# Performance work log

Measured on AMD Instinct MI355X. Metric: run time of the kernel, lower is better.

Reference implementation:

```python
import jax, jax.numpy as jnp
import numpy as np

T_MAX = 20
NUM_HEADS = 8
COMPLEXITY_W = 0.3
LN_EPS = 1e-5


def _layernorm(h, g, b):
    mu = jnp.mean(h, axis=-1, keepdims=True)
    var = jnp.var(h, axis=-1, keepdims=True)
    return (h - mu) / jnp.sqrt(var + LN_EPS) * g + b


def _gate_mlp(x, W1, b1, g, be, W2, b2, W3, b3):
    # Linear -> LayerNorm -> ReLU -> (Dropout=id in eval) -> Linear -> ReLU -> Linear -> Sigmoid
    h = jax.nn.relu(_layernorm(x @ W1 + b1, g, be))
    h = jax.nn.relu(h @ W2 + b2)
    return jax.nn.sigmoid(h @ W3 + b3)


def _adaptive_windows(x, p):
    S = x.shape[1]
    gate = _gate_mlp(x, p['gW1'], p['gb1'], p['gg'], p['gbe'], p['gW2'], p['gb2'], p['gW3'], p['gb3'])
    comp = _gate_mlp(x, p['cW1'], p['cb1'], p['cg'], p['cbe'], p['cW2'], p['cb2'], p['cW3'], p['cb3'])
    pos = jnp.linspace(0.8, 1.2, S, dtype=x.dtype).reshape(1, -1, 1)
    score = ((1.0 - COMPLEXITY_W) * gate + COMPLEXITY_W * comp) * pos
    T_i = jnp.clip(jnp.ceil(score[..., 0] * T_MAX), 1, T_MAX).astype(jnp.int32)  # [B,S]
    return T_i


def _spike_sum(x, T_i, alpha, beta):
    # LIF recurrence over T_MAX steps; accumulate masked spikes. x: [B,S,E]
    z = jnp.zeros_like(x)

    def step(carry, t):
        v, i, acc = carry
        active = (t < T_i).astype(x.dtype)[..., None]  # [B,S,1]
        i = alpha * i + x * active
        v = beta * v + i
        s = (v >= 1.0).astype(x.dtype)
        v = v * (1.0 - s)  # v_reset = 0
        return (v, i, acc + s * active), None

    (_, _, acc), _ = jax.lax.scan(step, (z, z, z), jnp.arange(T_MAX))
    return acc


def _forward(x, params):
    B, S, E = x.shape
    H, D = NUM_HEADS, E // NUM_HEADS
    q = x @ params['Wq']
    k = x @ params['Wk']
    v = x @ params['Wv']
    T_i = _adaptive_windows(x, params)
    q_sum = _spike_sum(q, T_i, params['alpha_q'], params['beta_q'])
    k_sum = _spike_sum(k, T_i, params['alpha_k'], params['beta_k'])
    v_mean = _spike_sum(v, T_i, params['alpha_v'], params['beta_v']) / T_MAX
    q_sum = q_sum.reshape(B, S, H, D)
    k_sum = k_sum.reshape(B, S, H, D)
    v_mean = v_mean.reshape(B, S, H, D)
    scale = D ** -0.5
    scores = jnp.einsum('bihd,bjhd->bhij', q_sum, k_sum) * scale
    w = jax.nn.softmax(scores, axis=-1)
    out = jnp.einsum('bhij,bjhd->bihd', w, v_mean).reshape(B, S, E)
    return out @ params['Wo'] + params['bo']


def setup_inputs() -> dict:
    key = jax.random.key(0)
    ks = iter(jax.random.split(key, 32))
    B, S, E = 4, 1024, 512
    f32 = jnp.float32

    def w(shape, scale=0.02):
        return jax.random.normal(next(ks), shape, dtype=f32) * scale

    inp = {
        'x': jax.random.normal(next(ks), (B, S, E), dtype=f32),
        'Wq': w((E, E)), 'Wk': w((E, E)), 'Wv': w((E, E)),
        'Wo': w((E, E)), 'bo': jnp.zeros((E,), f32),
        'gW1': w((E, 128)), 'gb1': jnp.zeros((128,), f32),
        'gg': jnp.ones((128,), f32), 'gbe': jnp.zeros((128,), f32),
        'gW2': w((128, 64)), 'gb2': jnp.zeros((64,), f32),
        'gW3': w((64, 1)), 'gb3': jnp.zeros((1,), f32),
        'cW1': w((E, 64)), 'cb1': jnp.zeros((64,), f32),
        'cg': jnp.ones((64,), f32), 'cbe': jnp.zeros((64,), f32),
        'cW2': w((64, 32)), 'cb2': jnp.zeros((32,), f32),
        'cW3': w((32, 1)), 'cb3': jnp.zeros((1,), f32),
        'alpha_q': jnp.asarray(np.exp(-1 / 5.0), f32), 'beta_q': jnp.asarray(np.exp(-1 / 20.0), f32),
        'alpha_k': jnp.asarray(np.exp(-1 / 5.0), f32), 'beta_k': jnp.asarray(np.exp(-1 / 20.0), f32),
        'alpha_v': jnp.asarray(np.exp(-1 / 5.0), f32), 'beta_v': jnp.asarray(np.exp(-1 / 20.0), f32),
    }
    return inp


def reference(x, Wq, Wk, Wv, Wo, bo,
              gW1, gb1, gg, gbe, gW2, gb2, gW3, gb3,
              cW1, cb1, cg, cbe, cW2, cb2, cW3, cb3,
              alpha_q, beta_q, alpha_k, beta_k, alpha_v, beta_v):
    params = dict(Wq=Wq, Wk=Wk, Wv=Wv, Wo=Wo, bo=bo,
                  gW1=gW1, gb1=gb1, gg=gg, gbe=gbe, gW2=gW2, gb2=gb2, gW3=gW3, gb3=gb3,
                  cW1=cW1, cb1=cb1, cg=cg, cbe=cbe, cW2=cW2, cb2=cb2, cW3=cW3, cb3=cb3,
                  alpha_q=alpha_q, beta_q=beta_q, alpha_k=alpha_k, beta_k=beta_k,
                  alpha_v=alpha_v, beta_v=beta_v)
    return _forward(x, params)
```

## Files before the change

kernel.cpp:

```cpp
#include <hip/hip_runtime.h>
#include <math.h>

#define SEQ   1024
#define EMB   512
#define NROWS 4096
#define LDP   72
#define GROWS 4

typedef __attribute__((ext_vector_type(8))) short short8;
typedef __attribute__((ext_vector_type(4))) float float4v;

__device__ __forceinline__ float bf2f(unsigned short s) {
    union { float f; unsigned u; } x; x.u = ((unsigned)s) << 16; return x.f;
}
__device__ __forceinline__ unsigned short f2bf(float f) {
    union { float f; unsigned u; } x; x.f = f;
    unsigned r = x.u + 0x7fffu + ((x.u >> 16) & 1u);
    return (unsigned short)(r >> 16);
}

__device__ __forceinline__ void gld16(const unsigned short* g, short* l) {
    __builtin_amdgcn_global_load_lds(
        (__attribute__((address_space(1))) void*)(g),
        (__attribute__((address_space(3))) void*)(l), 16, 0, 0);
}

__device__ __forceinline__ void split3(float x, unsigned short& h, unsigned short& m, unsigned short& l) {
    union { float f; unsigned u; } a; a.f = x;
    const unsigned rh = a.u + 0x7fffu + ((a.u >> 16) & 1u);
    h = (unsigned short)(rh >> 16);
    union { float f; unsigned u; } hf; hf.u = rh & 0xffff0000u;
    const float r1 = x - hf.f;
    a.f = r1;
    const unsigned rm = a.u + 0x7fffu + ((a.u >> 16) & 1u);
    m = (unsigned short)(rm >> 16);
    union { float f; unsigned u; } mf; mf.u = rm & 0xffff0000u;
    const float r2 = r1 - mf.f;
    l = f2bf(r2);
}

template<int H1, int H2>
__device__ __forceinline__ double mlp_eval(
    const double xs[GROWS][EMB], double* h1, double* h2, double* red,
    double* mu_s, double* var_s,
    const float* __restrict__ W1, const float* __restrict__ b1,
    const float* __restrict__ gam, const float* __restrict__ bet,
    const float* __restrict__ W2, const float* __restrict__ b2,
    const float* __restrict__ W3, const float* __restrict__ b3,
    int tid, int myrow)
{
    constexpr int S  = 256 / H1;
    constexpr int KS = EMB / S;

    {
        const int col = tid % H1, sk = tid / H1;
        double acc[GROWS] = {0.0, 0.0, 0.0, 0.0};
        const int kbeg = sk * KS;
        #pragma unroll 4
        for (int k = kbeg; k < kbeg + KS; ++k) {
            const double w = (double)W1[k * H1 + col];
            #pragma unroll
            for (int r = 0; r < GROWS; ++r) acc[r] += w * xs[r][k];
        }
        #pragma unroll
        for (int r = 0; r < GROWS; ++r) red[(sk * GROWS + r) * H1 + col] = acc[r];
    }
    __syncthreads();
    for (int idx = tid; idx < GROWS * H1; idx += 256) {
        const int r = idx / H1, cc = idx % H1;
        double s = 0.0;
        #pragma unroll
        for (int t = 0; t < S; ++t) s += red[(t * GROWS + r) * H1 + cc];
        h1[r * H1 + cc] = s + (double)b1[cc];
    }
    __syncthreads();

    {
        const int w = tid >> 6, l = tid & 63;
        double s = 0.0;
        for (int c = l; c < H1; c += 64) s += h1[w * H1 + c];
        #pragma unroll
        for (int off = 32; off >= 1; off >>= 1) s += __shfl_xor(s, off);
        if (l == 0) mu_s[w] = s / (double)H1;
    }
    __syncthreads();
    {
        const int w = tid >> 6, l = tid & 63;
        const double mu = mu_s[w];
        double s = 0.0;
        for (int c = l; c < H1; c += 64) { const double d = h1[w * H1 + c] - mu; s += d * d; }
        #pragma unroll
        for (int off = 32; off >= 1; off >>= 1) s += __shfl_xor(s, off);
        if (l == 0) var_s[w] = s / (double)H1;
    }
    __syncthreads();
    for (int idx = tid; idx < GROWS * H1; idx += 256) {
        const int r = idx / H1, cc = idx % H1;
        double hn = (h1[r * H1 + cc] - mu_s[r]) / sqrt(var_s[r] + 1e-5) * (double)gam[cc] + (double)bet[cc];
        h1[r * H1 + cc] = hn > 0.0 ? hn : 0.0;
    }
    __syncthreads();

    {
        const int col = tid % H2;
        const int r   = tid / H2;
        if (r < GROWS) {
            double acc = (double)b2[col];
            for (int k = 0; k < H1; ++k)
                acc += (double)W2[k * H2 + col] * h1[r * H1 + k];
            h2[r * H2 + col] = acc > 0.0 ? acc : 0.0;
        }
    }
    __syncthreads();

    {
        const int w = tid >> 6, l = tid & 63;
        double s = 0.0;
        for (int c = l; c < H2; c += 64) s += h2[w * H2 + c] * (double)W3[c];
        #pragma unroll
        for (int off = 32; off >= 1; off >>= 1) s += __shfl_xor(s, off);
        if (l == 0) mu_s[w] = s;
    }
    __syncthreads();
    double ret = 0.0;
    if (myrow >= 0) {
        const double z = mu_s[myrow] + (double)b3[0];
        ret = 1.0 / (1.0 + exp(-z));
    }
    return ret;
}

__global__ __launch_bounds__(256) void gates_split_kernel(
    const float* __restrict__ x,
    const float* __restrict__ gW1, const float* __restrict__ gb1,
    const float* __restrict__ gg,  const float* __restrict__ gbe,
    const float* __restrict__ gW2, const float* __restrict__ gb2,
    const float* __restrict__ gW3, const float* __restrict__ gb3,
    const float* __restrict__ cW1, const float* __restrict__ cb1,
    const float* __restrict__ cg,  const float* __restrict__ cbe,
    const float* __restrict__ cW2, const float* __restrict__ cb2,
    const float* __restrict__ cW3, const float* __restrict__ cb3,
    double* __restrict__ scores)
{
    __shared__ double xs[GROWS][EMB];
    __shared__ double h1[GROWS * 128];
    __shared__ double h2[GROWS * 64];
    __shared__ double red[1024];
    __shared__ double mu_s[GROWS], var_s[GROWS];

    const int row0 = blockIdx.x * GROWS;
    const int tid = threadIdx.x;

    for (int idx = tid; idx < GROWS * EMB; idx += 256) {
        const int r = idx >> 9, cc = idx & 511;
        xs[r][cc] = (double)x[(size_t)(row0 + r) * EMB + cc];
    }
    __syncthreads();

    const int myrow = (tid < GROWS) ? tid : -1;
    double v;
    if (blockIdx.y == 0)
        v = mlp_eval<128, 64>(xs, h1, h2, red, mu_s, var_s,
                              gW1, gb1, gg, gbe, gW2, gb2, gW3, gb3, tid, myrow);
    else
        v = mlp_eval<64, 32>(xs, h1, h2, red, mu_s, var_s,
                             cW1, cb1, cg, cbe, cW2, cb2, cW3, cb3, tid, myrow);

    if (myrow >= 0)
        scores[(size_t)blockIdx.y * NROWS + row0 + myrow] = v;
}

__global__ __launch_bounds__(256) void w_limbs_prep(
    const float* __restrict__ Wq, const float* __restrict__ Wk, const float* __restrict__ Wv,
    unsigned short* __restrict__ WL)
{
    const int z = blockIdx.z;
    const float* __restrict__ W = (z == 0) ? Wq : (z == 1) ? Wk : Wv;
    unsigned short* __restrict__ Th = WL + (size_t)z * 3 * EMB * EMB;
    unsigned short* __restrict__ Tm = Th + (size_t)EMB * EMB;
    unsigned short* __restrict__ Tl = Tm + (size_t)EMB * EMB;

    __shared__ __align__(16) float Ws[64][68];
    const int k0 = blockIdx.y * 64, n0 = blockIdx.x * 64;
    const int t = threadIdx.x;
    #pragma unroll
    for (int it = 0; it < 4; ++it) {
        const int idx = it * 256 + t;
        const int r = idx >> 4, c4 = (idx & 15) * 4;
        *(float4*)&Ws[r][c4] = *(const float4*)&W[(size_t)(k0 + r) * EMB + n0 + c4];
    }
    __syncthreads();
    #pragma unroll
    for (int it = 0; it < 2; ++it) {
        const int idx = it * 256 + t;
        const int n = idx >> 3, k8 = (idx & 7) * 8;
        short8 ph, pm, pl;
        #pragma unroll
        for (int j = 0; j < 8; ++j) {
            unsigned short h, m, l;
            split3(Ws[k8 + j][n], h, m, l);
            ph[j] = (short)h; pm[j] = (short)m; pl[j] = (short)l;
        }
        const size_t o = (size_t)(n0 + n) * EMB + k0 + k8;
        *(short8*)&Th[o] = ph;
        *(short8*)&Tm[o] = pm;
        *(short8*)&Tl[o] = pl;
    }
}

__global__ __launch_bounds__(256) void x_limbs_prep(
    const float* __restrict__ x, unsigned short* __restrict__ XL)
{
    unsigned short* __restrict__ Xh = XL;
    unsigned short* __restrict__ Xm = XL + (size_t)NROWS * EMB;
    unsigned short* __restrict__ Xl = Xm + (size_t)NROWS * EMB;
    const size_t i0 = ((size_t)blockIdx.x * 256 + threadIdx.x) * 8;
    const float4 a0 = *(const float4*)&x[i0];
    const float4 a1 = *(const float4*)&x[i0 + 4];
    const float av8[8] = {a0.x, a0.y, a0.z, a0.w, a1.x, a1.y, a1.z, a1.w};
    short8 ph, pm, pl;
    #pragma unroll
    for (int e = 0; e < 8; ++e) {
        unsigned short h, m, l;
        split3(av8[e], h, m, l);
        ph[e] = (short)h; pm[e] = (short)m; pl[e] = (short)l;
    }
    *(short8*)&Xh[i0] = ph;
    *(short8*)&Xm[i0] = pm;
    *(short8*)&Xl[i0] = pl;
}

__global__ __launch_bounds__(256) void qkv_mfma_lif_kernel(
    const unsigned short* __restrict__ XL, const unsigned short* __restrict__ WL,
    const float* __restrict__ aq, const float* __restrict__ bq,
    const float* __restrict__ akp, const float* __restrict__ bkp,
    const float* __restrict__ av, const float* __restrict__ bv,
    const double* __restrict__ scores,
    unsigned short* __restrict__ q_sum, unsigned short* __restrict__ k_sum,
    unsigned short* __restrict__ v_mean)
{
    const int z = blockIdx.z;
    const unsigned short* __restrict__ WTh = WL + (size_t)z * 3 * EMB * EMB;
    const unsigned short* __restrict__ WTm = WTh + (size_t)EMB * EMB;
    const unsigned short* __restrict__ WTl = WTm + (size_t)EMB * EMB;
    const unsigned short* __restrict__ Xh = XL;
    const unsigned short* __restrict__ Xm = XL + (size_t)NROWS * EMB;
    const unsigned short* __restrict__ Xl = Xm + (size_t)NROWS * EMB;
    unsigned short* __restrict__ out = (z == 0) ? q_sum : (z == 1) ? k_sum : v_mean;
    const double alpha = (double)((z == 0) ? aq : (z == 1) ? akp : av)[0];
    const double beta  = (double)((z == 0) ? bq : (z == 1) ? bkp : bv)[0];

    const int phys = blockIdx.x + 8 * blockIdx.y;
    const int logical = (phys & 7) * 32 + (phys >> 3);
    const int bx = logical & 7, by = logical >> 3;
    const int row0 = by * 128, col0 = bx * 64;

    __shared__ __align__(16) short As[3][128 * 32];
    __shared__ __align__(16) short Bs[3][64 * 32];

    const int tid  = threadIdx.x;
    const int lane = tid & 63, wave = tid >> 6;
    const int qd = lane >> 4, c = lane & 15;
    const int wrow = wave * 32;

    const int kc8 = ((lane & 3) ^ ((lane >> 3) & 3)) * 8;
    const size_t ga0 = (size_t)(row0 + wave * 16 + (lane >> 2)) * EMB + kc8;
    const size_t ga1 = ga0 + (size_t)64 * EMB;
    const size_t gb  = (size_t)(col0 + wave * 16 + (lane >> 2)) * EMB + kc8;

    int arf[2], brf[4];
    #pragma unroll
    for (int i = 0; i < 2; ++i) {
        const int Ra = wrow + i * 16 + c;
        arf[i] = Ra * 32 + ((qd ^ ((Ra >> 1) & 3)) * 8);
    }
    #pragma unroll
    for (int j = 0; j < 4; ++j) {
        const int Rb = j * 16 + c;
        brf[j] = Rb * 32 + ((qd ^ ((Rb >> 1) & 3)) * 8);
    }

    float4v acc[2][4];
    #pragma unroll
    for (int i = 0; i < 2; ++i)
        #pragma unroll
        for (int j = 0; j < 4; ++j)
            acc[i][j] = (float4v){0.f, 0.f, 0.f, 0.f};

    for (int k0 = 0; k0 < EMB; k0 += 32) {
        __syncthreads();
        gld16(Xh  + ga0 + k0, &As[0][wave * 512]);
        gld16(Xh  + ga1 + k0, &As[0][2048 + wave * 512]);
        gld16(Xm  + ga0 + k0, &As[1][wave * 512]);
        gld16(Xm  + ga1 + k0, &As[1][2048 + wave * 512]);
        gld16(Xl  + ga0 + k0, &As[2][wave * 512]);
        gld16(Xl  + ga1 + k0, &As[2][2048 + wave * 512]);
        gld16(WTh + gb  + k0, &Bs[0][wave * 512]);
        gld16(WTm + gb  + k0, &Bs[1][wave * 512]);
        gld16(WTl + gb  + k0, &Bs[2][wave * 512]);
        __syncthreads();

        short8 Afh[2], Afm[2], Afl[2];
        #pragma unroll
        for (int i = 0; i < 2; ++i) {
            Afh[i] = *(const short8*)&As[0][arf[i]];
            Afm[i] = *(const short8*)&As[1][arf[i]];
            Afl[i] = *(const short8*)&As[2][arf[i]];
        }
        short8 Bfh[4], Bfm[4], Bfl[4];
        #pragma unroll
        for (int j = 0; j < 4; ++j) {
            Bfh[j] = *(const short8*)&Bs[0][brf[j]];
            Bfm[j] = *(const short8*)&Bs[1][brf[j]];
            Bfl[j] = *(const short8*)&Bs[2][brf[j]];
        }

        #pragma unroll
        for (int i = 0; i < 2; ++i)
            #pragma unroll
            for (int j = 0; j < 4; ++j) {
                float4v t = acc[i][j];
                t = __builtin_amdgcn_mfma_f32_16x16x32_bf16(Afh[i], Bfh[j], t, 0, 0, 0);
                t = __builtin_amdgcn_mfma_f32_16x16x32_bf16(Afh[i], Bfm[j], t, 0, 0, 0);
                t = __builtin_amdgcn_mfma_f32_16x16x32_bf16(Afm[i], Bfh[j], t, 0, 0, 0);
                t = __builtin_amdgcn_mfma_f32_16x16x32_bf16(Afm[i], Bfm[j], t, 0, 0, 0);
                t = __builtin_amdgcn_mfma_f32_16x16x32_bf16(Afh[i], Bfl[j], t, 0, 0, 0);
                t = __builtin_amdgcn_mfma_f32_16x16x32_bf16(Afl[i], Bfh[j], t, 0, 0, 0);
                acc[i][j] = t;
            }
    }

    #pragma unroll
    for (int i = 0; i < 2; ++i)
        #pragma unroll
        for (int r = 0; r < 4; ++r) {
            const int gm = row0 + wrow + i * 16 + qd * 4 + r;
            const double g0 = scores[gm];
            const double c0 = scores[NROWS + gm];
            const int s = gm & (SEQ - 1);
            const double step = (1.2 - 0.8) / (double)(SEQ - 1);
            const double pos  = (double)s * step + 0.8;
            const double score = ((1.0 - 0.3) * g0 + 0.3 * c0) * pos;
            double td = ceil(score * 20.0);
            td = td < 1.0 ? 1.0 : (td > 20.0 ? 20.0 : td);
            const int T = (int)td;
            double cur0 = 0.0, cur1 = 0.0, cur2 = 0.0, cur3 = 0.0;
            double vm0 = 0.0, vm1 = 0.0, vm2 = 0.0, vm3 = 0.0;
            double sp0 = 0.0, sp1 = 0.0, sp2 = 0.0, sp3 = 0.0;
            const double xv0 = (double)acc[i][0][r];
            const double xv1 = (double)acc[i][1][r];
            const double xv2 = (double)acc[i][2][r];
            const double xv3 = (double)acc[i][3][r];
            for (int t = 0; t < T; ++t) {
                cur0 = alpha * cur0 + xv0; vm0 = beta * vm0 + cur0;
                if (vm0 >= 1.0) { sp0 += 1.0; vm0 = 0.0; }
                cur1 = alpha * cur1 + xv1; vm1 = beta * vm1 + cur1;
                if (vm1 >= 1.0) { sp1 += 1.0; vm1 = 0.0; }
                cur2 = alpha * cur2 + xv2; vm2 = beta * vm2 + cur2;
                if (vm2 >= 1.0) { sp2 += 1.0; vm2 = 0.0; }
                cur3 = alpha * cur3 + xv3; vm3 = beta * vm3 + cur3;
                if (vm3 >= 1.0) { sp3 += 1.0; vm3 = 0.0; }
            }
            if (z == 2) { sp0 /= 20.0; sp1 /= 20.0; sp2 /= 20.0; sp3 /= 20.0; }
            const size_t ob = (size_t)gm * EMB + col0 + c;
            out[ob +  0] = f2bf((float)sp0);
            out[ob + 16] = f2bf((float)sp1);
            out[ob + 32] = f2bf((float)sp2);
            out[ob + 48] = f2bf((float)sp3);
        }
}

__global__ __launch_bounds__(256) void attn_mfma_kernel(
    const unsigned short* __restrict__ q, const unsigned short* __restrict__ k,
    const unsigned short* __restrict__ v, unsigned short* __restrict__ attn_bf)
{
    __shared__ __align__(16) short Ks[64 * LDP];
    __shared__ __align__(16) short Pt[64 * LDP];
    __shared__ __align__(16) short Vt[64 * LDP];

    const int b = blockIdx.z, h = blockIdx.y;
    const int i0 = blockIdx.x * 64;
    const int tid  = threadIdx.x;
    const int wave = tid >> 6, lane = tid & 63;
    const int quad = lane >> 4, c = lane & 15;

    const unsigned short* Qb = q + ((size_t)b * SEQ + i0) * EMB + h * 64;
    const unsigned short* Kb = k + (size_t)b * SEQ * EMB + h * 64;
    const unsigned short* Vb = v + (size_t)b * SEQ * EMB + h * 64;

    short8 qf[2];
    {
        const int qrow = wave * 16 + c;
        #pragma unroll
        for (int ks = 0; ks < 2; ++ks) {
            short8 raw = *(const short8*)(Qb + (size_t)qrow * EMB + ks * 32 + quad * 8);
            short8 sc8;
            #pragma unroll
            for (int j = 0; j < 8; ++j)
                sc8[j] = (short)f2bf(bf2f((unsigned short)raw[j]) * 0.125f);
            qf[ks] = sc8;
        }
    }

    float m_r[4], l_r[4];
    float4v o[4];
    #pragma unroll
    for (int r = 0; r < 4; ++r) { m_r[r] = -1e30f; l_r[r] = 0.f; }
    #pragma unroll
    for (int nb = 0; nb < 4; ++nb)
        #pragma unroll
        for (int r = 0; r < 4; ++r) o[nb][r] = 0.f;

    for (int jt = 0; jt < SEQ / 64; ++jt) {
        #pragma unroll
        for (int it = 0; it < 2; ++it) {
            const int idx = it * 256 + tid;
            const int row = idx >> 3, ch = idx & 7;
            short8 val = *(const short8*)(Kb + (size_t)(jt * 64 + row) * EMB + ch * 8);
            *(short8*)&Ks[row * LDP + ch * 8] = val;
        }
        __syncthreads();

        float sc[4][4];
        #pragma unroll
        for (int nb = 0; nb < 4; ++nb) {
            float4v acc = {0.f, 0.f, 0.f, 0.f};
            #pragma unroll
            for (int ks = 0; ks < 2; ++ks) {
                short8 bfrag = *(const short8*)&Ks[(nb * 16 + c) * LDP + ks * 32 + quad * 8];
                acc = __builtin_amdgcn_mfma_f32_16x16x32_bf16(qf[ks], bfrag, acc, 0, 0, 0);
            }
            #pragma unroll
            for (int r = 0; r < 4; ++r) sc[nb][r] = acc[r];
        }

        float mnew[4], alpha[4];
        #pragma unroll
        for (int r = 0; r < 4; ++r) {
            float mx = fmaxf(fmaxf(sc[0][r], sc[1][r]), fmaxf(sc[2][r], sc[3][r]));
            #pragma unroll
            for (int off = 8; off >= 1; off >>= 1) mx = fmaxf(mx, __shfl_xor(mx, off));
            mnew[r]  = fmaxf(m_r[r], mx);
            alpha[r] = __expf(m_r[r] - mnew[r]);
            m_r[r]   = mnew[r];
        }
        float psum[4] = {0.f, 0.f, 0.f, 0.f};
        #pragma unroll
        for (int nb = 0; nb < 4; ++nb)
            #pragma unroll
            for (int r = 0; r < 4; ++r) {
                float p = __expf(sc[nb][r] - mnew[r]);
                psum[r] += p;
                Pt[(wave * 16 + quad * 4 + r) * LDP + nb * 16 + c] = (short)f2bf(p);
            }
        #pragma unroll
        for (int r = 0; r < 4; ++r) {
            float s = psum[r];
            #pragma unroll
            for (int off = 8; off >= 1; off >>= 1) s += __shfl_xor(s, off);
            l_r[r] = l_r[r] * alpha[r] + s;
            #pragma unroll
            for (int nb = 0; nb < 4; ++nb) o[nb][r] *= alpha[r];
        }

        {
            const int m = tid & 7, rp = tid >> 3;
            const int r = rp * 2;
            short8 v0 = *(const short8*)(Vb + (size_t)(jt * 64 + r) * EMB + m * 8);
            short8 v1 = *(const short8*)(Vb + (size_t)(jt * 64 + r + 1) * EMB + m * 8);
            const int rch = r >> 3, rlow = r & 7;
            #pragma unroll
            for (int i = 0; i < 8; ++i) {
                const int d = m * 8 + i;
                const int col = ((rch ^ m) << 3) + rlow;
                *(int*)&Vt[d * LDP + col] =
                    (int)((unsigned)(unsigned short)v0[i] |
                          ((unsigned)(unsigned short)v1[i] << 16));
            }
        }
        __syncthreads();

        short8 pf[2];
        #pragma unroll
        for (int ks = 0; ks < 2; ++ks)
            pf[ks] = *(const short8*)&Pt[(wave * 16 + c) * LDP + ks * 32 + quad * 8];
        #pragma unroll
        for (int nb = 0; nb < 4; ++nb) {
            float4v acc = o[nb];
            #pragma unroll
            for (int ks = 0; ks < 2; ++ks) {
                const int d = nb * 16 + c;
                const int kch = ks * 4 + quad;
                const int col = ((kch ^ (d >> 3)) << 3);
                short8 vfrag = *(const short8*)&Vt[d * LDP + col];
                acc = __builtin_amdgcn_mfma_f32_16x16x32_bf16(pf[ks], vfrag, acc, 0, 0, 0);
            }
            o[nb] = acc;
        }
    }

    #pragma unroll
    for (int r = 0; r < 4; ++r) {
        const float inv = 1.0f / l_r[r];
        const int row = i0 + wave * 16 + quad * 4 + r;
        #pragma unroll
        for (int nb = 0; nb < 4; ++nb)
            attn_bf[((size_t)b * SEQ + row) * EMB + h * 64 + nb * 16 + c] =
                f2bf(o[nb][r] * inv);
    }
}

__global__ __launch_bounds__(256) void wot_prep(
    const float* __restrict__ Wo, unsigned short* __restrict__ BT)
{
    __shared__ unsigned short Ws[64][72];
    const int k0 = blockIdx.y * 64, n0 = blockIdx.x * 64;
    const int t = threadIdx.x;
    #pragma unroll
    for (int it = 0; it < 4; ++it) {
        const int idx = it * 256 + t;
        const int r = idx >> 4, c4 = (idx & 15) * 4;
        const float4 w4 = *(const float4*)&Wo[(size_t)(k0 + r) * EMB + n0 + c4];
        Ws[r][c4 + 0] = f2bf(w4.x); Ws[r][c4 + 1] = f2bf(w4.y);
        Ws[r][c4 + 2] = f2bf(w4.z); Ws[r][c4 + 3] = f2bf(w4.w);
    }
    __syncthreads();
    #pragma unroll
    for (int it = 0; it < 2; ++it) {
        const int idx = it * 256 + t;
        const int n = idx >> 3, k8 = (idx & 7) * 8;
        short8 pack;
        #pragma unroll
        for (int j = 0; j < 8; ++j) pack[j] = (short)Ws[k8 + j][n];
        *(short8*)&BT[(size_t)(n0 + n) * EMB + k0 + k8] = pack;
    }
}

__global__ __launch_bounds__(256) void out_gemm_kernel(
    const unsigned short* __restrict__ A,
    const unsigned short* __restrict__ BT,
    const float* __restrict__ bias, float* __restrict__ out)
{
    const int tid  = threadIdx.x;
    const int lane = tid & 63, wave = tid >> 6;
    const int qd = lane >> 4, c = lane & 15;
    const int wm = (wave & 1) * 32, wn = (wave >> 1) * 32;
    const int row0 = blockIdx.y * 64, col0 = blockIdx.x * 64;

    float4v acc[2][2];
    #pragma unroll
    for (int i = 0; i < 2; ++i)
        #pragma unroll
        for (int j = 0; j < 2; ++j)
            acc[i][j] = (float4v){0.f, 0.f, 0.f, 0.f};

    for (int k0 = 0; k0 < EMB; k0 += 32) {
        short8 af[2], bf[2];
        #pragma unroll
        for (int i = 0; i < 2; ++i)
            af[i] = *(const short8*)&A[(size_t)(row0 + wm + i * 16 + c) * EMB + k0 + qd * 8];
        #pragma unroll
        for (int j = 0; j < 2; ++j)
            bf[j] = *(const short8*)&BT[(size_t)(col0 + wn + j * 16 + c) * EMB + k0 + qd * 8];
        #pragma unroll
        for (int i = 0; i < 2; ++i)
            #pragma unroll
            for (int j = 0; j < 2; ++j)
                acc[i][j] = __builtin_amdgcn_mfma_f32_16x16x32_bf16(af[i], bf[j], acc[i][j], 0, 0, 0);
    }

    #pragma unroll
    for (int i = 0; i < 2; ++i)
        #pragma unroll
        for (int r = 0; r < 4; ++r) {
            const int gm = row0 + wm + i * 16 + qd * 4 + r;
            #pragma unroll
            for (int j = 0; j < 2; ++j) {
                const int gn = col0 + wn + j * 16 + c;
                out[(size_t)gm * EMB + gn] = acc[i][j][r] + bias[gn];
            }
        }
}

extern "C" void kernel_launch(void* const* d_in, const int* in_sizes, int n_in,
                              void* d_out, int out_size, void* d_ws, size_t ws_size,
                              hipStream_t stream)
{
    const float* x   = (const float*)d_in[0];
    const float* Wq  = (const float*)d_in[1];
    const float* Wk  = (const float*)d_in[2];
    const float* Wv  = (const float*)d_in[3];
    const float* Wo  = (const float*)d_in[4];
    const float* bo  = (const float*)d_in[5];
    const float* gW1 = (const float*)d_in[6];
    const float* gb1 = (const float*)d_in[7];
    const float* gg  = (const float*)d_in[8];
    const float* gbe = (const float*)d_in[9];
    const float* gW2 = (const float*)d_in[10];
    const float* gb2 = (const float*)d_in[11];
    const float* gW3 = (const float*)d_in[12];
    const float* gb3 = (const float*)d_in[13];
    const float* cW1 = (const float*)d_in[14];
    const float* cb1 = (const float*)d_in[15];
    const float* cg  = (const float*)d_in[16];
    const float* cbe = (const float*)d_in[17];
    const float* cW2 = (const float*)d_in[18];
    const float* cb2 = (const float*)d_in[19];
    const float* cW3 = (const float*)d_in[20];
    const float* cb3 = (const float*)d_in[21];
    const float* aq  = (const float*)d_in[22];
    const float* bq  = (const float*)d_in[23];
    const float* ak  = (const float*)d_in[24];
    const float* bk  = (const float*)d_in[25];
    const float* av  = (const float*)d_in[26];
    const float* bv  = (const float*)d_in[27];

    unsigned short* q_sum   = (unsigned short*)((char*)d_ws + 16384);
    unsigned short* k_sum   = q_sum   + (size_t)NROWS * EMB;
    unsigned short* v_mean  = k_sum   + (size_t)NROWS * EMB;
    unsigned short* attn_bf = v_mean  + (size_t)NROWS * EMB;
    unsigned short* WoT     = attn_bf + (size_t)NROWS * EMB;
    unsigned short* WL      = WoT     + (size_t)EMB * EMB;
    unsigned short* XLp     = WL      + (size_t)9 * EMB * EMB;
    double* scores          = (double*)(XLp + (size_t)3 * NROWS * EMB);
    float* out = (float*)d_out;

    gates_split_kernel<<<dim3(NROWS / GROWS, 2), dim3(256), 0, stream>>>(
        x, gW1, gb1, gg, gbe, gW2, gb2, gW3, gb3,
        cW1, cb1, cg, cbe, cW2, cb2, cW3, cb3, scores);

    x_limbs_prep<<<dim3(NROWS * EMB / (256 * 8)), dim3(256), 0, stream>>>(x, XLp);

    w_limbs_prep<<<dim3(EMB / 64, EMB / 64, 3), dim3(256), 0, stream>>>(Wq, Wk, Wv, WL);

    qkv_mfma_lif_kernel<<<dim3(EMB / 64, NROWS / 128, 3), dim3(256), 0, stream>>>(
        XLp, WL, aq, bq, ak, bk, av, bv, scores, q_sum, k_sum, v_mean);

    wot_prep<<<dim3(EMB / 64, EMB / 64), dim3(256), 0, stream>>>(Wo, WoT);

    attn_mfma_kernel<<<dim3(SEQ / 64, 8, 4), dim3(256), 0, stream>>>(
        q_sum, k_sum, v_mean, attn_bf);

    out_gemm_kernel<<<dim3(EMB / 64, NROWS / 64), dim3(256), 0, stream>>>(
        attn_bf, WoT, bo, out);
}
```

Measured before the change: 269.4 us.

## Merge prep kernels into one launch and double-buffer QKV GEMM LDS staging

Four independent preprocessing kernels (gate MLPs, x limb split, Wq/Wk/Wv limb split, Wo transpose) now run as one launch, with the block index selecting the role. This removes three launches and the serialization gaps between them, and lets the heterogeneous blocks share the GPU. The QKV MFMA kernel also now double-buffers its LDS tiles, issuing the global-to-LDS load for the next K slice before computing on the current one. That halves the barriers per K step, at the cost of twice the LDS per block, which may lower occupancy.

```diff
diff --git a/kernel.cpp b/kernel.cpp
--- a/kernel.cpp
+++ b/kernel.cpp
@@ -130,7 +130,7 @@
     return ret;
 }
 
-__global__ __launch_bounds__(256) void gates_split_kernel(
+__global__ __launch_bounds__(256) void pre_kernel(
     const float* __restrict__ x,
     const float* __restrict__ gW1, const float* __restrict__ gb1,
     const float* __restrict__ gg,  const float* __restrict__ gbe,
@@ -140,94 +140,121 @@
     const float* __restrict__ cg,  const float* __restrict__ cbe,
     const float* __restrict__ cW2, const float* __restrict__ cb2,
     const float* __restrict__ cW3, const float* __restrict__ cb3,
-    double* __restrict__ scores)
+    double* __restrict__ scores,
+    const float* __restrict__ Wq, const float* __restrict__ Wk,
+    const float* __restrict__ Wv, unsigned short* __restrict__ WL,
+    unsigned short* __restrict__ XL,
+    const float* __restrict__ Wo, unsigned short* __restrict__ WoT)
 {
-    __shared__ double xs[GROWS][EMB];
-    __shared__ double h1[GROWS * 128];
-    __shared__ double h2[GROWS * 64];
-    __shared__ double red[1024];
-    __shared__ double mu_s[GROWS], var_s[GROWS];
-
-    const int row0 = blockIdx.x * GROWS;
+    __shared__ __align__(16) char smem[30784];
+    const int bid = blockIdx.x;
     const int tid = threadIdx.x;
 
-    for (int idx = tid; idx < GROWS * EMB; idx += 256) {
-        const int r = idx >> 9, cc = idx & 511;
-        xs[r][cc] = (double)x[(size_t)(row0 + r) * EMB + cc];
-    }
-    __syncthreads();
-
-    const int myrow = (tid < GROWS) ? tid : -1;
-    double v;
-    if (blockIdx.y == 0)
-        v = mlp_eval<128, 64>(xs, h1, h2, red, mu_s, var_s,
-                              gW1, gb1, gg, gbe, gW2, gb2, gW3, gb3, tid, myrow);
-    else
-        v = mlp_eval<64, 32>(xs, h1, h2, red, mu_s, var_s,
-                             cW1, cb1, cg, cbe, cW2, cb2, cW3, cb3, tid, myrow);
-
-    if (myrow >= 0)
-        scores[(size_t)blockIdx.y * NROWS + row0 + myrow] = v;
-}
-
-__global__ __launch_bounds__(256) void w_limbs_prep(
-    const float* __restrict__ Wq, const float* __restrict__ Wk, const float* __restrict__ Wv,
-    unsigned short* __restrict__ WL)
-{
-    const int z = blockIdx.z;
-    const float* __restrict__ W = (z == 0) ? Wq : (z == 1) ? Wk : Wv;
-    unsigned short* __restrict__ Th = WL + (size_t)z * 3 * EMB * EMB;
-    unsigned short* __restrict__ Tm = Th + (size_t)EMB * EMB;
-    unsigned short* __restrict__ Tl = Tm + (size_t)EMB * EMB;
-
-    __shared__ __align__(16) float Ws[64][68];
-    const int k0 = blockIdx.y * 64, n0 = blockIdx.x * 64;
-    const int t = threadIdx.x;
-    #pragma unroll
-    for (int it = 0; it < 4; ++it) {
-        const int idx = it * 256 + t;
-        const int r = idx >> 4, c4 = (idx & 15) * 4;
-        *(float4*)&Ws[r][c4] = *(const float4*)&W[(size_t)(k0 + r) * EMB + n0 + c4];
-    }
-    __syncthreads();
-    #pragma unroll
-    for (int it = 0; it < 2; ++it) {
-        const int idx = it * 256 + t;
-        const int n = idx >> 3, k8 = (idx & 7) * 8;
+    if (bid < 2048) {
+        double (*xs)[EMB] = (double(*)[EMB])smem;
+        double* h1    = (double*)(smem + 16384);
+        double* h2    = (double*)(smem + 20480);
+        double* red   = (double*)(smem + 22528);
+        double* mu_s  = (double*)(smem + 30720);
+        double* var_s = (double*)(smem + 30752);
+
+        const int gx = bid & 1023, gy = bid >> 10;
+        const int row0 = gx * GROWS;
+
+        for (int idx = tid; idx < GROWS * EMB; idx += 256) {
+            const int r = idx >> 9, cc = idx & 511;
+            xs[r][cc] = (double)x[(size_t)(row0 + r) * EMB + cc];
+        }
+        __syncthreads();
+
+        const int myrow = (tid < GROWS) ? tid : -1;
+        double v;
+        if (gy == 0)
+            v = mlp_eval<128, 64>(xs, h1, h2, red, mu_s, var_s,
+                                  gW1, gb1, gg, gbe, gW2, gb2, gW3, gb3, tid, myrow);
+        else
+            v = mlp_eval<64, 32>(xs, h1, h2, red, mu_s, var_s,
+                                 cW1, cb1, cg, cbe, cW2, cb2, cW3, cb3, tid, myrow);
+
+        if (myrow >= 0)
+            scores[(size_t)gy * NROWS + row0 + myrow] = v;
+
+    } else if (bid < 3072) {
+        unsigned short* Xh = XL;
+        unsigned short* Xm = XL + (size_t)NROWS * EMB;
+        unsigned short* Xl = Xm + (size_t)NROWS * EMB;
+        const size_t i0 = ((size_t)(bid - 2048) * 256 + tid) * 8;
+        const float4 a0 = *(const float4*)&x[i0];
+        const float4 a1 = *(const float4*)&x[i0 + 4];
+        const float av8[8] = {a0.x, a0.y, a0.z, a0.w, a1.x, a1.y, a1.z, a1.w};
         short8 ph, pm, pl;
         #pragma unroll
-        for (int j = 0; j < 8; ++j) {
+        for (int e = 0; e < 8; ++e) {
             unsigned short h, m, l;
-            split3(Ws[k8 + j][n], h, m, l);
-            ph[j] = (short)h; pm[j] = (short)m; pl[j] = (short)l;
-        }
-        const size_t o = (size_t)(n0 + n) * EMB + k0 + k8;
-        *(short8*)&Th[o] = ph;
-        *(short8*)&Tm[o] = pm;
-        *(short8*)&Tl[o] = pl;
-    }
-}
-
-__global__ __launch_bounds__(256) void x_limbs_prep(
-    const float* __restrict__ x, unsigned short* __restrict__ XL)
-{
-    unsigned short* __restrict__ Xh = XL;
-    unsigned short* __restrict__ Xm = XL + (size_t)NROWS * EMB;
-    unsigned short* __restrict__ Xl = Xm + (size_t)NROWS * EMB;
-    const size_t i0 = ((size_t)blockIdx.x * 256 + threadIdx.x) * 8;
-    const float4 a0 = *(const float4*)&x[i0];
-    const float4 a1 = *(const float4*)&x[i0 + 4];
-    const float av8[8] = {a0.x, a0.y, a0.z, a0.w, a1.x, a1.y, a1.z, a1.w};
-    short8 ph, pm, pl;
-    #pragma unroll
-    for (int e = 0; e < 8; ++e) {
-        unsigned short h, m, l;
-        split3(av8[e], h, m, l);
-        ph[e] = (short)h; pm[e] = (short)m; pl[e] = (short)l;
-    }
-    *(short8*)&Xh[i0] = ph;
-    *(short8*)&Xm[i0] = pm;
-    *(short8*)&Xl[i0] = pl;
+            split3(av8[e], h, m, l);
+            ph[e] = (short)h; pm[e] = (short)m; pl[e] = (short)l;
+        }
+        *(short8*)&Xh[i0] = ph;
+        *(short8*)&Xm[i0] = pm;
+        *(short8*)&Xl[i0] = pl;
+
+    } else if (bid < 3264) {
+        const int t = bid - 3072;
+        const int z = t >> 6, rem = t & 63;
+        const int k0 = (rem >> 3) * 64, n0 = (rem & 7) * 64;
+        const float* __restrict__ W = (z == 0) ? Wq : (z == 1) ? Wk : Wv;
+        unsigned short* Th = WL + (size_t)z * 3 * EMB * EMB;
+        unsigned short* Tm = Th + (size_t)EMB * EMB;
+        unsigned short* Tl = Tm + (size_t)EMB * EMB;
+
+        float (*Ws)[68] = (float(*)[68])smem;
+        #pragma unroll
+        for (int it = 0; it < 4; ++it) {
+            const int idx = it * 256 + tid;
+            const int r = idx >> 4, c4 = (idx & 15) * 4;
+            *(float4*)&Ws[r][c4] = *(const float4*)&W[(size_t)(k0 + r) * EMB + n0 + c4];
+        }
+        __syncthreads();
+        #pragma unroll
+        for (int it = 0; it < 2; ++it) {
+            const int idx = it * 256 + tid;
+            const int n = idx >> 3, k8 = (idx & 7) * 8;
+            short8 ph, pm, pl;
+            #pragma unroll
+            for (int j = 0; j < 8; ++j) {
+                unsigned short h, m, l;
+                split3(Ws[k8 + j][n], h, m, l);
+                ph[j] = (short)h; pm[j] = (short)m; pl[j] = (short)l;
+            }
+            const size_t o = (size_t)(n0 + n) * EMB + k0 + k8;
+            *(short8*)&Th[o] = ph;
+            *(short8*)&Tm[o] = pm;
+            *(short8*)&Tl[o] = pl;
+        }
+
+    } else {
+        const int t = bid - 3264;
+        const int k0 = (t >> 3) * 64, n0 = (t & 7) * 64;
+        unsigned short (*Ws)[72] = (unsigned short(*)[72])smem;
+        #pragma unroll
+        for (int it = 0; it < 4; ++it) {
+            const int idx = it * 256 + tid;
+            const int r = idx >> 4, c4 = (idx & 15) * 4;
+            const float4 w4 = *(const float4*)&Wo[(size_t)(k0 + r) * EMB + n0 + c4];
+            Ws[r][c4 + 0] = f2bf(w4.x); Ws[r][c4 + 1] = f2bf(w4.y);
+            Ws[r][c4 + 2] = f2bf(w4.z); Ws[r][c4 + 3] = f2bf(w4.w);
+        }
+        __syncthreads();
+        #pragma unroll
+        for (int it = 0; it < 2; ++it) {
+            const int idx = it * 256 + tid;
+            const int n = idx >> 3, k8 = (idx & 7) * 8;
+            short8 pack;
+            #pragma unroll
+            for (int j = 0; j < 8; ++j) pack[j] = (short)Ws[k8 + j][n];
+            *(short8*)&WoT[(size_t)(n0 + n) * EMB + k0 + k8] = pack;
+        }
+    }
 }
 
 __global__ __launch_bounds__(256) void qkv_mfma_lif_kernel(
@@ -255,8 +282,8 @@
     const int bx = logical & 7, by = logical >> 3;
     const int row0 = by * 128, col0 = bx * 64;
 
-    __shared__ __align__(16) short As[3][128 * 32];
-    __shared__ __align__(16) short Bs[3][64 * 32];
+    __shared__ __align__(16) short As0[3][4096], As1[3][4096];
+    __shared__ __align__(16) short Bs0[3][2048], Bs1[3][2048];
 
     const int tid  = threadIdx.x;
     const int lane = tid & 63, wave = tid >> 6;
@@ -287,34 +314,32 @@
         for (int j = 0; j < 4; ++j)
             acc[i][j] = (float4v){0.f, 0.f, 0.f, 0.f};
 
-    for (int k0 = 0; k0 < EMB; k0 += 32) {
-        __syncthreads();
-        gld16(Xh  + ga0 + k0, &As[0][wave * 512]);
-        gld16(Xh  + ga1 + k0, &As[0][2048 + wave * 512]);
-        gld16(Xm  + ga0 + k0, &As[1][wave * 512]);
-        gld16(Xm  + ga1 + k0, &As[1][2048 + wave * 512]);
-        gld16(Xl  + ga0 + k0, &As[2][wave * 512]);
-        gld16(Xl  + ga1 + k0, &As[2][2048 + wave * 512]);
-        gld16(WTh + gb  + k0, &Bs[0][wave * 512]);
-        gld16(WTm + gb  + k0, &Bs[1][wave * 512]);
-        gld16(WTl + gb  + k0, &Bs[2][wave * 512]);
-        __syncthreads();
-
+    auto STAGE = [&](short (*A_)[4096], short (*B_)[2048], int k0) {
+        gld16(Xh  + ga0 + k0, &A_[0][wave * 512]);
+        gld16(Xh  + ga1 + k0, &A_[0][2048 + wave * 512]);
+        gld16(Xm  + ga0 + k0, &A_[1][wave * 512]);
+        gld16(Xm  + ga1 + k0, &A_[1][2048 + wave * 512]);
+        gld16(Xl  + ga0 + k0, &A_[2][wave * 512]);
+        gld16(Xl  + ga1 + k0, &A_[2][2048 + wave * 512]);
+        gld16(WTh + gb  + k0, &B_[0][wave * 512]);
+        gld16(WTm + gb  + k0, &B_[1][wave * 512]);
+        gld16(WTl + gb  + k0, &B_[2][wave * 512]);
+    };
+    auto COMPUTE = [&](const short (*A_)[4096], const short (*B_)[2048]) {
         short8 Afh[2], Afm[2], Afl[2];
         #pragma unroll
         for (int i = 0; i < 2; ++i) {
-            Afh[i] = *(const short8*)&As[0][arf[i]];
-            Afm[i] = *(const short8*)&As[1][arf[i]];
-            Afl[i] = *(const short8*)&As[2][arf[i]];
+            Afh[i] = *(const short8*)&A_[0][arf[i]];
+            Afm[i] = *(const short8*)&A_[1][arf[i]];
+            Afl[i] = *(const short8*)&A_[2][arf[i]];
         }
         short8 Bfh[4], Bfm[4], Bfl[4];
         #pragma unroll
         for (int j = 0; j < 4; ++j) {
-            Bfh[j] = *(const short8*)&Bs[0][brf[j]];
-            Bfm[j] = *(const short8*)&Bs[1][brf[j]];
-            Bfl[j] = *(const short8*)&Bs[2][brf[j]];
-        }
-
+            Bfh[j] = *(const short8*)&B_[0][brf[j]];
+            Bfm[j] = *(const short8*)&B_[1][brf[j]];
+            Bfl[j] = *(const short8*)&B_[2][brf[j]];
+        }
         #pragma unroll
         for (int i = 0; i < 2; ++i)
             #pragma unroll
@@ -328,6 +353,17 @@
                 t = __builtin_amdgcn_mfma_f32_16x16x32_bf16(Afl[i], Bfh[j], t, 0, 0, 0);
                 acc[i][j] = t;
             }
+    };
+
+    STAGE(As0, Bs0, 0);
+    __syncthreads();
+    for (int k0 = 0; k0 < EMB; k0 += 64) {
+        STAGE(As1, Bs1, k0 + 32);
+        COMPUTE(As0, Bs0);
+        __syncthreads();
+        if (k0 + 64 < EMB) STAGE(As0, Bs0, k0 + 64);
+        COMPUTE(As1, Bs1);
+        __syncthreads();
     }
 
     #pragma unroll
@@ -507,32 +543,6 @@
         for (int nb = 0; nb < 4; ++nb)
             attn_bf[((size_t)b * SEQ + row) * EMB + h * 64 + nb * 16 + c] =
                 f2bf(o[nb][r] * inv);
-    }
-}
-
-__global__ __launch_bounds__(256) void wot_prep(
-    const float* __restrict__ Wo, unsigned short* __restrict__ BT)
-{
-    __shared__ unsigned short Ws[64][72];
-    const int k0 = blockIdx.y * 64, n0 = blockIdx.x * 64;
-    const int t = threadIdx.x;
-    #pragma unroll
-    for (int it = 0; it < 4; ++it) {
-        const int idx = it * 256 + t;
-        const int r = idx >> 4, c4 = (idx & 15) * 4;
-        const float4 w4 = *(const float4*)&Wo[(size_t)(k0 + r) * EMB + n0 + c4];
-        Ws[r][c4 + 0] = f2bf(w4.x); Ws[r][c4 + 1] = f2bf(w4.y);
-        Ws[r][c4 + 2] = f2bf(w4.z); Ws[r][c4 + 3] = f2bf(w4.w);
-    }
-    __syncthreads();
-    #pragma unroll
-    for (int it = 0; it < 2; ++it) {
-        const int idx = it * 256 + t;
-        const int n = idx >> 3, k8 = (idx & 7) * 8;
-        short8 pack;
-        #pragma unroll
-        for (int j = 0; j < 8; ++j) pack[j] = (short)Ws[k8 + j][n];
-        *(short8*)&BT[(size_t)(n0 + n) * EMB + k0 + k8] = pack;
     }
 }
 
@@ -625,19 +635,14 @@
     double* scores          = (double*)(XLp + (size_t)3 * NROWS * EMB);
     float* out = (float*)d_out;
 
-    gates_split_kernel<<<dim3(NROWS / GROWS, 2), dim3(256), 0, stream>>>(
+    pre_kernel<<<dim3(3328), dim3(256), 0, stream>>>(
         x, gW1, gb1, gg, gbe, gW2, gb2, gW3, gb3,
-        cW1, cb1, cg, cbe, cW2, cb2, cW3, cb3, scores);
-
-    x_limbs_prep<<<dim3(NROWS * EMB / (256 * 8)), dim3(256), 0, stream>>>(x, XLp);
-
-    w_limbs_prep<<<dim3(EMB / 64, EMB / 64, 3), dim3(256), 0, stream>>>(Wq, Wk, Wv, WL);
+        cW1, cb1, cg, cbe, cW2, cb2, cW3, cb3, scores,
+        Wq, Wk, Wv, WL, XLp, Wo, WoT);
 
     qkv_mfma_lif_kernel<<<dim3(EMB / 64, NROWS / 128, 3), dim3(256), 0, stream>>>(
         XLp, WL, aq, bq, ak, bk, av, bv, scores, q_sum, k_sum, v_mean);
 
-    wot_prep<<<dim3(EMB / 64, EMB / 64), dim3(256), 0, stream>>>(Wo, WoT);
-
     attn_mfma_kernel<<<dim3(SEQ / 64, 8, 4), dim3(256), 0, stream>>>(
         q_sum, k_sum, v_mean, attn_bf);
 
```

Result: no change. 264.4 us (-1.8%).
